# Performance work log

Measured on AMD Instinct MI355X. Metric: run time of the kernel, lower is better.

The kernel has to match this reference:

```python
import jax, jax.numpy as jnp
import numpy as np

B, FT, N, H = 1, 512, 4096, 4

def setup_inputs() -> dict:
    key = jax.random.key(0)
    k1, k2, k3, k4 = jax.random.split(key, 4)
    ft_mat = jax.random.normal(k1, (B, FT, N), dtype=jnp.float32)
    bias_mat = jax.random.normal(k2, (B, N, N), dtype=jnp.float32)
    # Conv1d(ft_dim, 1, 1) per head == per-head linear projection over channels
    W = jax.random.normal(k3, (H, FT), dtype=jnp.float32) * (1.0 / np.sqrt(FT))
    b = jax.random.normal(k4, (H,), dtype=jnp.float32) * 0.01
    return {"ft_mat": ft_mat, "bias_mat": bias_mat, "W": W, "b": b}

def reference(ft_mat, bias_mat, W, b):
    # per-head 1x1 conv: w[b,h,n] = sum_f W[h,f] * ft_mat[b,f,n] + b[h]
    w = jnp.einsum('hf,bfn->bhn', W, ft_mat) + b[None, :, None]
    # score[b,h,i,j] = w_i + w_j (w + w^T broadcast), then leaky_relu(0.2)
    s = jax.nn.leaky_relu(w[:, :, :, None] + w[:, :, None, :], negative_slope=0.2)
    # bias-mask softmax over last dim (dropout is identity in eval mode)
    a = jax.nn.softmax(s + bias_mat[:, None, :, :], axis=-1)
    # trans_ft = a @ a^T per head
    t = jnp.einsum('bhij,bhkj->bhik', a, a)
    # torch.cat(res_mat, dim=2): head blocks contiguous along last dim
    Bn, Hn, Nn, _ = t.shape
    return t.transpose(0, 2, 1, 3).reshape(Bn, Nn, Hn * Nn)
```

## Files before the change

kernel.cpp:

```cpp
#include <hip/hip_runtime.h>
#include <hip/hip_bf16.h>

#define N_DIM 4096
#define FT_DIM 512
#define H_DIM 4
#define OUT_LD (H_DIM * N_DIM)

typedef __attribute__((ext_vector_type(8))) __bf16 bf16x8;
typedef __attribute__((ext_vector_type(4))) float f32x4;
typedef unsigned int u32;
typedef unsigned short u16;

__device__ inline float bf2f(u16 u) {
    u32 x = ((u32)u) << 16;
    return __uint_as_float(x);
}
__device__ inline u16 f2bf_rn(float f) {
    u32 x = __float_as_uint(f);
    u32 r = x + 0x7fffu + ((x >> 16) & 1u);
    return (u16)(r >> 16);
}

__device__ inline void gload16(const void* g, void* l) {
    __builtin_amdgcn_global_load_lds(
        (const __attribute__((address_space(1))) u32*)g,
        (__attribute__((address_space(3))) u32*)l, 16, 0, 0);
}

__global__ __launch_bounds__(256) void wproj_kernel(
    const float* __restrict__ ft, const float* __restrict__ W,
    const float* __restrict__ bvec, float* __restrict__ wout) {
    int n = blockIdx.x * 256 + threadIdx.x;
    float a0 = 0.f, a1 = 0.f, a2 = 0.f, a3 = 0.f;
#pragma unroll 8
    for (int f = 0; f < FT_DIM; ++f) {
        float v = ft[(size_t)f * N_DIM + n];
        a0 = fmaf(W[0 * FT_DIM + f], v, a0);
        a1 = fmaf(W[1 * FT_DIM + f], v, a1);
        a2 = fmaf(W[2 * FT_DIM + f], v, a2);
        a3 = fmaf(W[3 * FT_DIM + f], v, a3);
    }
    wout[0 * N_DIM + n] = a0 + bvec[0];
    wout[1 * N_DIM + n] = a1 + bvec[1];
    wout[2 * N_DIM + n] = a2 + bvec[2];
    wout[3 * N_DIM + n] = a3 + bvec[3];
}

__global__ __launch_bounds__(256) void softmax_split_kernel(
    const float* __restrict__ w, const float* __restrict__ bias,
    u16* __restrict__ ahi, u16* __restrict__ alo) {
    const int i = blockIdx.x;
    const int t = threadIdx.x;
    __shared__ float red[8];

    float bj[16];
    const float4* b4 = (const float4*)(bias + (size_t)i * N_DIM);
#pragma unroll
    for (int c = 0; c < 4; ++c) {
        float4 v = b4[t + 256 * c];
        bj[c * 4 + 0] = v.x;
        bj[c * 4 + 1] = v.y;
        bj[c * 4 + 2] = v.z;
        bj[c * 4 + 3] = v.w;
    }

    for (int h = 0; h < H_DIM; ++h) {
        __syncthreads();
        const float wi = w[h * N_DIM + i];
        const float4* w4 = (const float4*)(w + h * N_DIM);

        float l[16];
        float m = -1e30f;
#pragma unroll
        for (int c = 0; c < 4; ++c) {
            float4 wj = w4[t + 256 * c];
            float x;
            x = wi + wj.x; x = (x >= 0.f) ? x : 0.2f * x; x += bj[c * 4 + 0]; l[c * 4 + 0] = x;
            x = wi + wj.y; x = (x >= 0.f) ? x : 0.2f * x; x += bj[c * 4 + 1]; l[c * 4 + 1] = x;
            x = wi + wj.z; x = (x >= 0.f) ? x : 0.2f * x; x += bj[c * 4 + 2]; l[c * 4 + 2] = x;
            x = wi + wj.w; x = (x >= 0.f) ? x : 0.2f * x; x += bj[c * 4 + 3]; l[c * 4 + 3] = x;
            m = fmaxf(m, fmaxf(fmaxf(l[c * 4 + 0], l[c * 4 + 1]),
                               fmaxf(l[c * 4 + 2], l[c * 4 + 3])));
        }
#pragma unroll
        for (int o = 32; o > 0; o >>= 1) m = fmaxf(m, __shfl_xor(m, o, 64));
        if ((t & 63) == 0) red[t >> 6] = m;
        __syncthreads();
        m = fmaxf(fmaxf(red[0], red[1]), fmaxf(red[2], red[3]));

        float p[16];
        float s = 0.f;
#pragma unroll
        for (int k = 0; k < 16; ++k) {
            float e = __expf(l[k] - m);
            p[k] = e;
            s += e;
        }
#pragma unroll
        for (int o = 32; o > 0; o >>= 1) s += __shfl_xor(s, o, 64);
        if ((t & 63) == 0) red[4 + (t >> 6)] = s;
        __syncthreads();
        s = (red[4] + red[5]) + (red[6] + red[7]);
        float inv = 1.0f / s;

        u16* hrow = ahi + ((size_t)(h * N_DIM + i)) * N_DIM;
        u16* lrow = alo + ((size_t)(h * N_DIM + i)) * N_DIM;
#pragma unroll
        for (int c = 0; c < 4; ++c) {
            int j0 = (t + 256 * c) * 4;
            ushort4 hv, lv;
            float av;
            av = p[c * 4 + 0] * inv; hv.x = f2bf_rn(av); lv.x = f2bf_rn(av - bf2f(hv.x));
            av = p[c * 4 + 1] * inv; hv.y = f2bf_rn(av); lv.y = f2bf_rn(av - bf2f(hv.y));
            av = p[c * 4 + 2] * inv; hv.z = f2bf_rn(av); lv.z = f2bf_rn(av - bf2f(hv.z));
            av = p[c * 4 + 3] * inv; hv.w = f2bf_rn(av); lv.w = f2bf_rn(av - bf2f(hv.w));
            *(ushort4*)(hrow + j0) = hv;
            *(ushort4*)(lrow + j0) = lv;
        }
    }
}

__global__ __launch_bounds__(256, 2) void aat_mfma_kernel(
    const u16* __restrict__ Ahi, const u16* __restrict__ Alo,
    float* __restrict__ out) {
    const int bx = blockIdx.x;
    const int lin = (bx & 7) * 66 + (bx >> 3);
    int idx = lin, tI = 0, base = 0;
    while (idx >= base + (32 - tI)) { base += (32 - tI); ++tI; }
    const int tK = tI + (idx - base);
    const int h = blockIdx.y;

    const int t = threadIdx.x;
    const int l = t & 63;
    const int wv = t >> 6;
    const int wr = wv >> 1, wc = wv & 1;
    const int lr = l & 15, c16 = l >> 4;

    __shared__ __align__(16) unsigned char smem[32768];

    const size_t headoff = (size_t)h * N_DIM * N_DIM;
    const char* baseP[4];
    baseP[0] = (const char*)(Ahi + headoff + (size_t)(tI * 128) * N_DIM);
    baseP[1] = (const char*)(Ahi + headoff + (size_t)(tK * 128) * N_DIM);
    baseP[2] = (const char*)(Alo + headoff + (size_t)(tI * 128) * N_DIM);
    baseP[3] = (const char*)(Alo + headoff + (size_t)(tK * 128) * N_DIM);

    u32 goff[2], loff[2];
#pragma unroll
    for (int hh = 0; hh < 2; ++hh) {
        int chunk = hh * 256 + t;
        int row = chunk >> 2;
        int cc = (chunk & 3) ^ ((row >> 1) & 3);
        goff[hh] = (u32)row * (N_DIM * 2) + (u32)cc * 16;
        loff[hh] = (u32)chunk * 16;
    }

    u32 offA[2][4], offB[2][4];
#pragma unroll
    for (int m = 0; m < 4; ++m) {
        int rowA = wr * 64 + m * 16 + lr;
        u32 oa = (u32)rowA * 64 + (u32)((c16 ^ ((rowA >> 1) & 3)) * 16);
        offA[0][m] = 0 * 8192 + oa;
        offA[1][m] = 2 * 8192 + oa;
        int rowB = wc * 64 + m * 16 + lr;
        u32 ob = (u32)rowB * 64 + (u32)((c16 ^ ((rowB >> 1) & 3)) * 16);
        offB[0][m] = 1 * 8192 + ob;
        offB[1][m] = 3 * 8192 + ob;
    }

    f32x4 acc[4][4];
#pragma unroll
    for (int m = 0; m < 4; ++m)
#pragma unroll
        for (int n = 0; n < 4; ++n) acc[m][n] = (f32x4){0.f, 0.f, 0.f, 0.f};

    for (int kt = 0; kt < N_DIM; kt += 32) {
        __syncthreads();
        const u32 ktb = (u32)kt * 2;
#pragma unroll
        for (int tt = 0; tt < 4; ++tt) {
            gload16(baseP[tt] + ktb + goff[0], smem + tt * 8192 + loff[0]);
            gload16(baseP[tt] + ktb + goff[1], smem + tt * 8192 + loff[1]);
        }
        __syncthreads();

        bf16x8 aU[4], aL[4], bU[4], bL[4];
#pragma unroll
        for (int m = 0; m < 4; ++m) {
            aU[m] = *(const bf16x8*)(smem + offA[0][m]);
            aL[m] = *(const bf16x8*)(smem + offA[1][m]);
            bU[m] = *(const bf16x8*)(smem + offB[0][m]);
            bL[m] = *(const bf16x8*)(smem + offB[1][m]);
        }
#pragma unroll
        for (int m = 0; m < 4; ++m)
#pragma unroll
            for (int n = 0; n < 4; ++n) {
                acc[m][n] = __builtin_amdgcn_mfma_f32_16x16x32_bf16(
                    aU[m], bU[n], acc[m][n], 0, 0, 0);
                acc[m][n] = __builtin_amdgcn_mfma_f32_16x16x32_bf16(
                    aU[m], bL[n], acc[m][n], 0, 0, 0);
                acc[m][n] = __builtin_amdgcn_mfma_f32_16x16x32_bf16(
                    aL[m], bU[n], acc[m][n], 0, 0, 0);
            }
    }

    float* oh = out + (size_t)h * N_DIM;
    const int orow0 = tI * 128 + wr * 64;
    const int ocol0 = tK * 128 + wc * 64;
#pragma unroll
    for (int m = 0; m < 4; ++m)
#pragma unroll
        for (int n = 0; n < 4; ++n) {
            int r0 = orow0 + m * 16 + c16 * 4;
            int cc0 = ocol0 + n * 16 + lr;
            oh[(size_t)(r0 + 0) * OUT_LD + cc0] = acc[m][n][0];
            oh[(size_t)(r0 + 1) * OUT_LD + cc0] = acc[m][n][1];
            oh[(size_t)(r0 + 2) * OUT_LD + cc0] = acc[m][n][2];
            oh[(size_t)(r0 + 3) * OUT_LD + cc0] = acc[m][n][3];
        }

    if (tI != tK) {
#pragma unroll
        for (int m = 0; m < 4; ++m)
#pragma unroll
            for (int n = 0; n < 4; ++n) {
                int rm = tK * 128 + wc * 64 + n * 16 + lr;
                int cm = tI * 128 + wr * 64 + m * 16 + c16 * 4;
                *(f32x4*)(oh + (size_t)rm * OUT_LD + cm) = acc[m][n];
            }
    }
}

extern "C" void kernel_launch(void* const* d_in, const int* in_sizes, int n_in,
                              void* d_out, int out_size, void* d_ws,
                              size_t ws_size, hipStream_t stream) {
    const float* ft = (const float*)d_in[0];
    const float* bias = (const float*)d_in[1];
    const float* W = (const float*)d_in[2];
    const float* bvec = (const float*)d_in[3];
    float* out = (float*)d_out;

    float* wbuf = (float*)d_ws;
    const size_t a_elems = (size_t)H_DIM * N_DIM * N_DIM;
    u16* ahi = (u16*)((char*)d_ws + 65536);
    u16* alo = (u16*)((char*)d_ws + 65536 + a_elems * 2);

    wproj_kernel<<<dim3(16), dim3(256), 0, stream>>>(ft, W, bvec, wbuf);
    softmax_split_kernel<<<dim3(N_DIM), dim3(256), 0, stream>>>(wbuf, bias,
                                                                ahi, alo);
    const int ntiles = 32 * 33 / 2;
    aat_mfma_kernel<<<dim3(ntiles, H_DIM), dim3(256), 0, stream>>>(ahi, alo,
                                                                   out);
}
```

Before: 1.377 ms.

## Enlarge A·Aᵀ MFMA tiles to 256x256 with double-buffered LDS prefetch

Moves the symmetric A·Aᵀ GEMM from 128x128 tiles with 256 threads to 256x256 tiles with 512 threads, eight waves each owning a 128x64 sub-tile. The k-loop now double-buffers the hi/lo bf16 slabs in 128KB of LDS: the next k-slice is issued through global_load_lds while the current one is consumed. The loop also uses inline ds_read_b128, explicit waitcnt and barriers, and s_setprio around the MFMA bursts. The aim is to raise data reuse per LDS and global byte and to hide load latency behind MFMA work. In exchange, the grid shrinks to 544 blocks at one block per CU, which risks tail imbalance, and register pressure rises with the 8x4 accumulators.

```diff
diff --git a/kernel.cpp b/kernel.cpp
--- a/kernel.cpp
+++ b/kernel.cpp
@@ -5,6 +5,7 @@
 #define FT_DIM 512
 #define H_DIM 4
 #define OUT_LD (H_DIM * N_DIM)
+#define NTILES 128
 
 typedef __attribute__((ext_vector_type(8))) __bf16 bf16x8;
 typedef __attribute__((ext_vector_type(4))) float f32x4;
@@ -25,6 +26,16 @@
     __builtin_amdgcn_global_load_lds(
         (const __attribute__((address_space(1))) u32*)g,
         (__attribute__((address_space(3))) u32*)l, 16, 0, 0);
+}
+
+__device__ inline u32 lds_addr(const void* p) {
+    return (u32)(size_t)(const __attribute__((address_space(3))) void*)p;
+}
+
+__device__ inline bf16x8 dsr128(u32 addr) {
+    bf16x8 d;
+    asm volatile("ds_read_b128 %0, %1" : "=v"(d) : "v"(addr));
+    return d;
 }
 
 __global__ __launch_bounds__(256) void wproj_kernel(
@@ -120,114 +131,146 @@
     }
 }
 
-__global__ __launch_bounds__(256, 2) void aat_mfma_kernel(
+__global__ __launch_bounds__(512, 2) void aat_mfma_kernel(
     const u16* __restrict__ Ahi, const u16* __restrict__ Alo,
     float* __restrict__ out) {
     const int bx = blockIdx.x;
-    const int lin = (bx & 7) * 66 + (bx >> 3);
+    const int lin = (bx & 7) * 17 + (bx >> 3);
     int idx = lin, tI = 0, base = 0;
-    while (idx >= base + (32 - tI)) { base += (32 - tI); ++tI; }
+    while (idx >= base + (16 - tI)) { base += (16 - tI); ++tI; }
     const int tK = tI + (idx - base);
     const int h = blockIdx.y;
 
     const int t = threadIdx.x;
     const int l = t & 63;
     const int wv = t >> 6;
-    const int wr = wv >> 1, wc = wv & 1;
+    const int wr = wv >> 2;
+    const int wc = wv & 3;
     const int lr = l & 15, c16 = l >> 4;
 
-    __shared__ __align__(16) unsigned char smem[32768];
+    __shared__ __align__(16) unsigned char smem[131072];
+    const u32 sbase = lds_addr(smem);
 
     const size_t headoff = (size_t)h * N_DIM * N_DIM;
     const char* baseP[4];
-    baseP[0] = (const char*)(Ahi + headoff + (size_t)(tI * 128) * N_DIM);
-    baseP[1] = (const char*)(Ahi + headoff + (size_t)(tK * 128) * N_DIM);
-    baseP[2] = (const char*)(Alo + headoff + (size_t)(tI * 128) * N_DIM);
-    baseP[3] = (const char*)(Alo + headoff + (size_t)(tK * 128) * N_DIM);
-
-    u32 goff[2], loff[2];
-#pragma unroll
-    for (int hh = 0; hh < 2; ++hh) {
-        int chunk = hh * 256 + t;
-        int row = chunk >> 2;
-        int cc = (chunk & 3) ^ ((row >> 1) & 3);
-        goff[hh] = (u32)row * (N_DIM * 2) + (u32)cc * 16;
-        loff[hh] = (u32)chunk * 16;
-    }
-
-    u32 offA[2][4], offB[2][4];
-#pragma unroll
-    for (int m = 0; m < 4; ++m) {
-        int rowA = wr * 64 + m * 16 + lr;
-        u32 oa = (u32)rowA * 64 + (u32)((c16 ^ ((rowA >> 1) & 3)) * 16);
-        offA[0][m] = 0 * 8192 + oa;
-        offA[1][m] = 2 * 8192 + oa;
-        int rowB = wc * 64 + m * 16 + lr;
-        u32 ob = (u32)rowB * 64 + (u32)((c16 ^ ((rowB >> 1) & 3)) * 16);
-        offB[0][m] = 1 * 8192 + ob;
-        offB[1][m] = 3 * 8192 + ob;
-    }
-
-    f32x4 acc[4][4];
-#pragma unroll
-    for (int m = 0; m < 4; ++m)
-#pragma unroll
-        for (int n = 0; n < 4; ++n) acc[m][n] = (f32x4){0.f, 0.f, 0.f, 0.f};
-
-    for (int kt = 0; kt < N_DIM; kt += 32) {
-        __syncthreads();
-        const u32 ktb = (u32)kt * 2;
-#pragma unroll
-        for (int tt = 0; tt < 4; ++tt) {
-            gload16(baseP[tt] + ktb + goff[0], smem + tt * 8192 + loff[0]);
-            gload16(baseP[tt] + ktb + goff[1], smem + tt * 8192 + loff[1]);
-        }
-        __syncthreads();
-
-        bf16x8 aU[4], aL[4], bU[4], bL[4];
-#pragma unroll
-        for (int m = 0; m < 4; ++m) {
-            aU[m] = *(const bf16x8*)(smem + offA[0][m]);
-            aL[m] = *(const bf16x8*)(smem + offA[1][m]);
-            bU[m] = *(const bf16x8*)(smem + offB[0][m]);
-            bL[m] = *(const bf16x8*)(smem + offB[1][m]);
-        }
-#pragma unroll
-        for (int m = 0; m < 4; ++m)
-#pragma unroll
-            for (int n = 0; n < 4; ++n) {
-                acc[m][n] = __builtin_amdgcn_mfma_f32_16x16x32_bf16(
-                    aU[m], bU[n], acc[m][n], 0, 0, 0);
-                acc[m][n] = __builtin_amdgcn_mfma_f32_16x16x32_bf16(
-                    aU[m], bL[n], acc[m][n], 0, 0, 0);
-                acc[m][n] = __builtin_amdgcn_mfma_f32_16x16x32_bf16(
-                    aL[m], bU[n], acc[m][n], 0, 0, 0);
-            }
+    baseP[0] = (const char*)(Ahi + headoff + (size_t)(tI * 256) * N_DIM);
+    baseP[1] = (const char*)(Alo + headoff + (size_t)(tI * 256) * N_DIM);
+    baseP[2] = (const char*)(Ahi + headoff + (size_t)(tK * 256) * N_DIM);
+    baseP[3] = (const char*)(Alo + headoff + (size_t)(tK * 256) * N_DIM);
+
+    u32 gsoff[2];
+#pragma unroll
+    for (int s2 = 0; s2 < 2; ++s2) {
+        int pc = t + 512 * s2;
+        int row = pc >> 2;
+        int cc = (pc & 3) ^ ((row >> 1) & 3);
+        gsoff[s2] = (u32)row * (N_DIM * 2) + (u32)cc * 16;
+    }
+    const u32 lbase = (u32)t * 16;
+
+    u32 oAU[8], oAL[8], oBU[4], oBL[4];
+#pragma unroll
+    for (int mi = 0; mi < 8; ++mi) {
+        int r = wr * 128 + mi * 16 + lr;
+        u32 o = (u32)r * 64 + (u32)((c16 ^ ((r >> 1) & 3)) * 16);
+        oAU[mi] = sbase + o;
+        oAL[mi] = sbase + 16384 + o;
+    }
+#pragma unroll
+    for (int ni = 0; ni < 4; ++ni) {
+        int r = wc * 64 + ni * 16 + lr;
+        u32 o = (u32)r * 64 + (u32)((c16 ^ ((r >> 1) & 3)) * 16);
+        oBU[ni] = sbase + 32768 + o;
+        oBL[ni] = sbase + 49152 + o;
+    }
+
+    f32x4 acc[8][4];
+#pragma unroll
+    for (int mi = 0; mi < 8; ++mi)
+#pragma unroll
+        for (int ni = 0; ni < 4; ++ni) acc[mi][ni] = (f32x4){0.f, 0.f, 0.f, 0.f};
+
+#pragma unroll
+    for (int j = 0; j < 8; ++j)
+        gload16(baseP[j >> 1] + gsoff[j & 1], smem + (lbase + j * 8192));
+    asm volatile("s_waitcnt vmcnt(0)" ::: "memory");
+    __builtin_amdgcn_sched_barrier(0);
+    __builtin_amdgcn_s_barrier();
+
+    for (int tk = 0; tk < NTILES; ++tk) {
+        const u32 curoff = (u32)(tk & 1) << 16;
+        const u32 nxtoff = curoff ^ 65536u;
+        bf16x8 bU[4], bL[4];
+#pragma unroll
+        for (int q = 0; q < 4; ++q) {
+            if (q == 0) {
+#pragma unroll
+                for (int ni = 0; ni < 4; ++ni) {
+                    bU[ni] = dsr128(oBU[ni] + curoff);
+                    bL[ni] = dsr128(oBL[ni] + curoff);
+                }
+            }
+            bf16x8 aU0 = dsr128(oAU[2 * q + 0] + curoff);
+            bf16x8 aU1 = dsr128(oAU[2 * q + 1] + curoff);
+            bf16x8 aL0 = dsr128(oAL[2 * q + 0] + curoff);
+            bf16x8 aL1 = dsr128(oAL[2 * q + 1] + curoff);
+            if (q == 0 && tk < NTILES - 1) {
+                const u32 ktb = (u32)(tk + 1) * 64;
+#pragma unroll
+                for (int j = 0; j < 8; ++j)
+                    gload16(baseP[j >> 1] + ktb + gsoff[j & 1],
+                            smem + (nxtoff + lbase + j * 8192));
+            }
+            __builtin_amdgcn_s_barrier();
+            asm volatile("s_waitcnt lgkmcnt(0)" ::: "memory");
+            __builtin_amdgcn_sched_barrier(0);
+            __builtin_amdgcn_s_setprio(1);
+#pragma unroll
+            for (int m2 = 0; m2 < 2; ++m2) {
+                const bf16x8 au = m2 ? aU1 : aU0;
+                const bf16x8 al = m2 ? aL1 : aL0;
+#pragma unroll
+                for (int ni = 0; ni < 4; ++ni) {
+                    acc[2 * q + m2][ni] = __builtin_amdgcn_mfma_f32_16x16x32_bf16(
+                        au, bU[ni], acc[2 * q + m2][ni], 0, 0, 0);
+                    acc[2 * q + m2][ni] = __builtin_amdgcn_mfma_f32_16x16x32_bf16(
+                        au, bL[ni], acc[2 * q + m2][ni], 0, 0, 0);
+                    acc[2 * q + m2][ni] = __builtin_amdgcn_mfma_f32_16x16x32_bf16(
+                        al, bU[ni], acc[2 * q + m2][ni], 0, 0, 0);
+                }
+            }
+            __builtin_amdgcn_s_setprio(0);
+            if (q == 3) {
+                asm volatile("s_waitcnt vmcnt(0)" ::: "memory");
+                __builtin_amdgcn_sched_barrier(0);
+            }
+            __builtin_amdgcn_s_barrier();
+        }
     }
 
     float* oh = out + (size_t)h * N_DIM;
-    const int orow0 = tI * 128 + wr * 64;
-    const int ocol0 = tK * 128 + wc * 64;
-#pragma unroll
-    for (int m = 0; m < 4; ++m)
-#pragma unroll
-        for (int n = 0; n < 4; ++n) {
-            int r0 = orow0 + m * 16 + c16 * 4;
-            int cc0 = ocol0 + n * 16 + lr;
-            oh[(size_t)(r0 + 0) * OUT_LD + cc0] = acc[m][n][0];
-            oh[(size_t)(r0 + 1) * OUT_LD + cc0] = acc[m][n][1];
-            oh[(size_t)(r0 + 2) * OUT_LD + cc0] = acc[m][n][2];
-            oh[(size_t)(r0 + 3) * OUT_LD + cc0] = acc[m][n][3];
+    const int r0b = tI * 256 + wr * 128;
+    const int c0b = tK * 256 + wc * 64;
+#pragma unroll
+    for (int mi = 0; mi < 8; ++mi)
+#pragma unroll
+        for (int ni = 0; ni < 4; ++ni) {
+            int r0 = r0b + mi * 16 + c16 * 4;
+            int cc0 = c0b + ni * 16 + lr;
+            oh[(size_t)(r0 + 0) * OUT_LD + cc0] = acc[mi][ni][0];
+            oh[(size_t)(r0 + 1) * OUT_LD + cc0] = acc[mi][ni][1];
+            oh[(size_t)(r0 + 2) * OUT_LD + cc0] = acc[mi][ni][2];
+            oh[(size_t)(r0 + 3) * OUT_LD + cc0] = acc[mi][ni][3];
         }
 
     if (tI != tK) {
 #pragma unroll
-        for (int m = 0; m < 4; ++m)
-#pragma unroll
-            for (int n = 0; n < 4; ++n) {
-                int rm = tK * 128 + wc * 64 + n * 16 + lr;
-                int cm = tI * 128 + wr * 64 + m * 16 + c16 * 4;
-                *(f32x4*)(oh + (size_t)rm * OUT_LD + cm) = acc[m][n];
+        for (int mi = 0; mi < 8; ++mi)
+#pragma unroll
+            for (int ni = 0; ni < 4; ++ni) {
+                int rm = c0b + ni * 16 + lr;
+                int cm = r0b + mi * 16 + c16 * 4;
+                *(f32x4*)(oh + (size_t)rm * OUT_LD + cm) = acc[mi][ni];
             }
     }
 }
@@ -249,7 +292,7 @@
     wproj_kernel<<<dim3(16), dim3(256), 0, stream>>>(ft, W, bvec, wbuf);
     softmax_split_kernel<<<dim3(N_DIM), dim3(256), 0, stream>>>(wbuf, bias,
                                                                 ahi, alo);
-    const int ntiles = 32 * 33 / 2;
-    aat_mfma_kernel<<<dim3(ntiles, H_DIM), dim3(256), 0, stream>>>(ahi, alo,
+    const int ntiles = 16 * 17 / 2;
+    aat_mfma_kernel<<<dim3(ntiles, H_DIM), dim3(512), 0, stream>>>(ahi, alo,
                                                                    out);
 }
```

Result: no change. 1.383 ms (+0.4%).
